# Performance work log

Measured on AMD Instinct MI355X. Metric: run time of the kernel, lower is better.

## Reference

```python
import jax, jax.numpy as jnp
import numpy as np

B, S, H = 8, 2048, 2048


def setup_inputs() -> dict:
    key = jax.random.key(0)
    k1, k2, k3 = jax.random.split(key, 3)
    hidden_state = jax.random.normal(k1, (B, S, H), dtype=jnp.float32)
    attention_mask = jnp.ones((B, S), dtype=jnp.int32)
    special_embeddings_mask = jnp.zeros((B, S), dtype=jnp.int32).at[:, 0].set(1)
    # torch samples -log(Exp(1)) == standard Gumbel; pass noise explicitly for determinism
    gumbel_noise = jax.random.gumbel(k2, (B, S, 2), dtype=jnp.float32)
    W = jax.random.normal(k3, (2 * H, 2), dtype=jnp.float32) / np.sqrt(2.0 * H)
    b = jnp.zeros((2,), dtype=jnp.float32)
    return {"hidden_state": hidden_state, "attention_mask": attention_mask,
            "special_embeddings_mask": special_embeddings_mask,
            "gumbel_noise": gumbel_noise, "W": W, "b": b}


def _forward(hidden_state, W, b, gumbel_noise, attention_mask, special_embeddings_mask):
    Bs, Ss, Hs = hidden_state.shape
    mask_b = attention_mask.astype(bool)
    # adjacent pair features [h_i, h_{i+1}], zero stub appended at the last position
    pairs = jnp.concatenate([hidden_state[:, :-1], hidden_state[:, 1:]], axis=-1)
    pairs = jnp.concatenate([pairs, jnp.zeros((Bs, 1, 2 * Hs), pairs.dtype)], axis=1)
    logits = pairs @ W + b  # [B,S,2]
    # hard Gumbel-softmax with straight-through estimator (tau=1, scale=1, invert=False)
    y_soft = jax.nn.softmax(logits + gumbel_noise, axis=-1)
    index = jnp.argmax(y_soft, axis=-1)
    y_hard = jax.nn.one_hot(index, 2, dtype=logits.dtype)
    mm = y_hard - jax.lax.stop_gradient(y_soft) + y_soft
    # special tokens never merge; padded positions contribute nothing
    mm = jnp.where(special_embeddings_mask.astype(bool)[..., None],
                   jnp.asarray([1.0, 0.0], mm.dtype), mm)
    mm = mm * mask_b[..., None].astype(mm.dtype)
    # ---- vectorized run-length merge (replaces the serial per-batch python loop) ----
    idx = jnp.arange(Ss)
    T = jnp.sum(attention_mask, axis=-1).astype(jnp.int32)  # valid token counts [B]
    valid = idx[None, :] < T[:, None]  # [B,S]
    # a position participates in a merge run iff it votes merge and 1 <= i < T-1
    want = (mm[..., 1] > 0.5) & (idx[None, :] >= 1) & (idx[None, :] < (T[:, None] - 1))
    want_prev = jnp.pad(want[:, :-1], ((0, 0), (1, 0)))
    # new output row starts unless position continues an existing merge run
    inc = (valid & (idx[None, :] >= 1) & ~(want & want_prev)).astype(jnp.int32)
    r = jnp.cumsum(inc, axis=-1)  # destination output row for each input position
    v = jnp.where(want, mm[..., 1], mm[..., 0])
    v = jnp.where(idx[None, :] == 0, jnp.asarray(1.0, v.dtype), v)  # transform[:,0,0] = 1
    v = jnp.where(valid, v, jnp.asarray(0.0, v.dtype))
    b_idx = jnp.arange(Bs)[:, None]
    transform = jnp.zeros((Bs, Ss, Ss), hidden_state.dtype).at[b_idx, r, idx[None, :]].add(v)
    counts = jnp.zeros((Bs, Ss), hidden_state.dtype).at[b_idx, r].add(valid.astype(hidden_state.dtype))
    new_len = r[:, -1] + 1  # merged sequence length per row
    merged_attention_mask = (idx[None, :] < new_len[:, None]).astype(hidden_state.dtype)
    merged_special = jnp.zeros((Bs, Ss), hidden_state.dtype).at[:, 0].set(1.0)
    merged_special = merged_special.at[jnp.arange(Bs), new_len - 1].set(1.0)
    merged_hidden = jnp.einsum('bts,bsh->bth', transform, hidden_state)
    return merged_hidden, merged_attention_mask, merged_special, counts, mm, logits


def reference(hidden_state, attention_mask, special_embeddings_mask, gumbel_noise, W, b):
    return _forward(hidden_state, W, b, gumbel_noise, attention_mask, special_embeddings_mask)
```

## Files before the change

### kernel.cpp

```cpp
#include <hip/hip_runtime.h>
#include <math.h>

#define Bq 8
#define Sq 2048
#define Hq 2048
#define BSq (Bq*Sq)

#define OFF_MH  ((size_t)0)
#define OFF_MAM ((size_t)BSq*Hq)
#define OFF_MSP (OFF_MAM + (size_t)BSq)
#define OFF_CNT (OFF_MSP + (size_t)BSq)
#define OFF_MM  (OFF_CNT + (size_t)BSq)
#define OFF_LG  (OFF_MM + (size_t)2*BSq)

#define WS_DOTS 0
#define WS_V    ((size_t)BSq*16)
#define WS_SEG  (WS_V + (size_t)BSq*4)
#define WS_META (WS_SEG + (size_t)BSq*4)

typedef float nfloat4 __attribute__((ext_vector_type(4)));

__device__ inline float4 f4add(float4 a, float4 b) {
  return make_float4(a.x+b.x, a.y+b.y, a.z+b.z, a.w+b.w);
}

__device__ inline void nt_store_f4(float4 v, float4* p) {
  nfloat4 nv;
  nv.x = v.x; nv.y = v.y; nv.z = v.z; nv.w = v.w;
  __builtin_nontemporal_store(nv, (nfloat4*)p);
}

__global__ __launch_bounds__(256) void k1_dots(const float* __restrict__ hid,
                                               const float* __restrict__ Wg,
                                               float4* __restrict__ dots) {
  __shared__ float4 part[4][256];
  const int tid = threadIdx.x;
  const float4* W4 = (const float4*)Wg;
  const float4 wa0 = W4[2*tid],           wa1 = W4[2*tid+1];
  const float4 wa2 = W4[2*(256+tid)],     wa3 = W4[2*(256+tid)+1];
  const float4 wb0 = W4[1024+2*tid],      wb1 = W4[1024+2*tid+1];
  const float4 wb2 = W4[1024+2*(256+tid)],wb3 = W4[1024+2*(256+tid)+1];
  const int base = blockIdx.x * 16;
  for (int tk0 = 0; tk0 < 16; tk0 += 4) {
    #pragma unroll
    for (int j = 0; j < 4; ++j) {
      const float4* hr = (const float4*)(hid + (size_t)(base + tk0 + j) * Hq);
      float4 h0 = hr[tid], h1 = hr[256+tid];
      float d0 = h0.x*wa0.x + h0.y*wa0.z + h0.z*wa1.x + h0.w*wa1.z
               + h1.x*wa2.x + h1.y*wa2.z + h1.z*wa3.x + h1.w*wa3.z;
      float d1 = h0.x*wa0.y + h0.y*wa0.w + h0.z*wa1.y + h0.w*wa1.w
               + h1.x*wa2.y + h1.y*wa2.w + h1.z*wa3.y + h1.w*wa3.w;
      float e0 = h0.x*wb0.x + h0.y*wb0.z + h0.z*wb1.x + h0.w*wb1.z
               + h1.x*wb2.x + h1.y*wb2.z + h1.z*wb3.x + h1.w*wb3.z;
      float e1 = h0.x*wb0.y + h0.y*wb0.w + h0.z*wb1.y + h0.w*wb1.w
               + h1.x*wb2.y + h1.y*wb2.w + h1.z*wb3.y + h1.w*wb3.w;
      part[j][tid] = make_float4(d0, d1, e0, e1);
    }
    __syncthreads();
    const int w = tid >> 6, l = tid & 63;
    float4 s = f4add(f4add(part[w][l], part[w][l+64]),
                     f4add(part[w][l+128], part[w][l+192]));
    #pragma unroll
    for (int off = 32; off > 0; off >>= 1) {
      s.x += __shfl_xor(s.x, off);
      s.y += __shfl_xor(s.y, off);
      s.z += __shfl_xor(s.z, off);
      s.w += __shfl_xor(s.w, off);
    }
    if (l == 0) dots[base + tk0 + w] = s;
    __syncthreads();
  }
}

__global__ __launch_bounds__(256) void k2_merge(const float4* __restrict__ dots,
                                                const int* __restrict__ attn,
                                                const int* __restrict__ spec,
                                                const float* __restrict__ gum,
                                                const float* __restrict__ bias,
                                                float* __restrict__ out,
                                                float* __restrict__ v_ws,
                                                int* __restrict__ seg_ws,
                                                int* __restrict__ meta) {
  const int b = blockIdx.x, tid = threadIdx.x;
  __shared__ int sums[256];
  __shared__ unsigned char wantL[Sq];
  __shared__ int seg[Sq];
  __shared__ int sT;
  const float b0 = bias[0], b1 = bias[1];

  int tsum = 0;
  #pragma unroll
  for (int k = 0; k < 8; ++k) tsum += attn[b*Sq + tid*8 + k];
  sums[tid] = tsum; __syncthreads();
  for (int off = 128; off > 0; off >>= 1) {
    if (tid < off) sums[tid] += sums[tid+off];
    __syncthreads();
  }
  if (tid == 0) sT = sums[0];
  __syncthreads();
  const int T = sT;

  int wloc[8];
  #pragma unroll
  for (int k = 0; k < 8; ++k) {
    const int i  = tid*8 + k;
    const int gi = b*Sq + i;
    float4 di = dots[gi];
    float l0, l1;
    if (i < Sq-1) {
      float4 dn = dots[gi+1];
      l0 = (di.x + dn.z) + b0;
      l1 = (di.y + dn.w) + b1;
    } else { l0 = b0; l1 = b1; }
    out[OFF_LG + (size_t)gi*2 + 0] = l0;
    out[OFF_LG + (size_t)gi*2 + 1] = l1;
    float z0 = l0 + gum[(size_t)gi*2 + 0];
    float z1 = l1 + gum[(size_t)gi*2 + 1];
    float m  = fmaxf(z0, z1);
    float e0 = expf(z0 - m), e1 = expf(z1 - m);
    float den = e0 + e1;
    float p0 = e0 / den, p1 = e1 / den;
    int idx1 = (p1 > p0) ? 1 : 0;
    float h0f = idx1 ? 0.0f : 1.0f, h1f = idx1 ? 1.0f : 0.0f;
    float mm0 = (h0f - p0) + p0;
    float mm1 = (h1f - p1) + p1;
    if (spec[gi] != 0) { mm0 = 1.0f; mm1 = 0.0f; }
    float am = (float)attn[gi];
    mm0 *= am; mm1 *= am;
    out[OFF_MM + (size_t)gi*2 + 0] = mm0;
    out[OFF_MM + (size_t)gi*2 + 1] = mm1;
    int want = (mm1 > 0.5f) && (i >= 1) && (i < T-1);
    wantL[i] = (unsigned char)want;
    wloc[k]  = want;
    float v = want ? mm1 : mm0;
    if (i == 0) v = 1.0f;
    if (i >= T) v = 0.0f;
    v_ws[gi] = v;
  }
  __syncthreads();

  int incs[8]; int run = 0;
  #pragma unroll
  for (int k = 0; k < 8; ++k) {
    const int i = tid*8 + k;
    int wprev = (i >= 1) ? (int)wantL[i-1] : 0;
    int inc = (i < T && i >= 1 && !(wloc[k] && wprev)) ? 1 : 0;
    run += inc;
    incs[k] = run;
  }
  sums[tid] = run; __syncthreads();
  for (int off = 1; off < 256; off <<= 1) {
    int val = (tid >= off) ? sums[tid - off] : 0;
    __syncthreads();
    sums[tid] += val;
    __syncthreads();
  }
  const int excl = sums[tid] - run;
  const int total = sums[255];

  if (tid == 0) seg[0] = 0;
  #pragma unroll
  for (int k = 0; k < 8; ++k) {
    const int i = tid*8 + k;
    int inc = (k == 0) ? incs[0] : (incs[k] - incs[k-1]);
    if (inc) seg[excl + incs[k]] = i;
  }
  __syncthreads();

  const int nl = total + 1;
  if (tid == 0) { meta[b*2] = nl; meta[b*2+1] = T; }

  #pragma unroll
  for (int k = 0; k < 8; ++k) {
    const int t  = tid*8 + k;
    const int gi = b*Sq + t;
    seg_ws[gi] = (t < nl) ? seg[t] : 0;
    float cnt = 0.0f, mam = 0.0f, msp = 0.0f;
    if (t < nl) {
      int s0 = seg[t];
      int s1 = (t+1 < nl) ? seg[t+1] : T;
      cnt = (float)(s1 - s0);
      mam = 1.0f;
    }
    if (t == 0 || t == nl-1) msp = 1.0f;
    out[OFF_MAM + gi] = mam;
    out[OFF_MSP + gi] = msp;
    out[OFF_CNT + gi] = cnt;
  }
}

#define K3_ROWS 16
__global__ __launch_bounds__(256) void k3_gather(const float* __restrict__ hid,
                                                 const float* __restrict__ v_ws,
                                                 const int* __restrict__ seg_ws,
                                                 const int* __restrict__ meta,
                                                 float* __restrict__ out_mh) {
  const int blocksPerBatch = Sq / K3_ROWS;
  const int b  = blockIdx.x / blocksPerBatch;
  const int t0 = (blockIdx.x % blocksPerBatch) * K3_ROWS;
  const int tid = threadIdx.x;
  const int nl = meta[b*2];
  const int T  = meta[b*2+1];

  __shared__ int bound[K3_ROWS + 1];
  if (tid <= K3_ROWS) {
    const int t = t0 + tid;
    bound[tid] = (t < nl) ? seg_ws[b*Sq + t] : T;
  }
  __syncthreads();

  const int rbase = b*Sq;
  int i = bound[0];
  #pragma unroll 1
  for (int r = 0; r < K3_ROWS; ++r) {
    float4 a0 = make_float4(0.f,0.f,0.f,0.f), a1 = a0;
    const int s1 = bound[r+1];
    for (; i < s1; ++i) {
      const float w = v_ws[rbase + i];
      const float4* hr = (const float4*)(hid + (size_t)(rbase + i) * Hq);
      const float4 x0 = hr[tid];
      const float4 x1 = hr[256 + tid];
      a0.x = fmaf(w, x0.x, a0.x); a0.y = fmaf(w, x0.y, a0.y);
      a0.z = fmaf(w, x0.z, a0.z); a0.w = fmaf(w, x0.w, a0.w);
      a1.x = fmaf(w, x1.x, a1.x); a1.y = fmaf(w, x1.y, a1.y);
      a1.z = fmaf(w, x1.z, a1.z); a1.w = fmaf(w, x1.w, a1.w);
    }
    float4* orow = (float4*)(out_mh + (size_t)(rbase + t0 + r) * Hq);
    nt_store_f4(a0, orow + tid);
    nt_store_f4(a1, orow + 256 + tid);
  }
}

extern "C" void kernel_launch(void* const* d_in, const int* in_sizes, int n_in,
                              void* d_out, int out_size, void* d_ws, size_t ws_size,
                              hipStream_t stream) {
  (void)in_sizes; (void)n_in; (void)out_size; (void)ws_size;
  const float* hid  = (const float*)d_in[0];
  const int*   attn = (const int*)d_in[1];
  const int*   spec = (const int*)d_in[2];
  const float* gum  = (const float*)d_in[3];
  const float* Wg   = (const float*)d_in[4];
  const float* bias = (const float*)d_in[5];
  float* out = (float*)d_out;
  char*  ws  = (char*)d_ws;
  float4* dots  = (float4*)(ws + WS_DOTS);
  float* v_ws   = (float*)(ws + WS_V);
  int*   seg_ws = (int*)(ws + WS_SEG);
  int*   meta   = (int*)(ws + WS_META);

  k1_dots<<<dim3(BSq/16), dim3(256), 0, stream>>>(hid, Wg, dots);
  k2_merge<<<dim3(Bq), dim3(256), 0, stream>>>(dots, attn, spec, gum, bias,
                                               out, v_ws, seg_ws, meta);
  k3_gather<<<dim3(Bq*(Sq/K3_ROWS)), dim3(256), 0, stream>>>(hid, v_ws, seg_ws,
                                                             meta, out + OFF_MH);
}
```

Before: 274.0 us.

## Fuse dots, merge and gather into one cooperative kernel with grid syncs

Turns the three kernels into device phase functions and runs them from a single cooperative kernel of 1024 blocks. Two grid.sync barriers separate the dot, merge and gather phases, which removes two kernel launch boundaries and their drain and refill gaps. In exchange, all 1024 blocks must stay resident (launch_bounds 256,4), and most of them sit idle at the barrier while the 8 merge blocks run. If the cooperative launch fails, it falls back to the original three launches.

```diff
diff --git a/kernel.cpp b/kernel.cpp
--- a/kernel.cpp
+++ b/kernel.cpp
@@ -1,10 +1,15 @@
 #include <hip/hip_runtime.h>
+#include <hip/hip_cooperative_groups.h>
 #include <math.h>
+
+namespace cg = cooperative_groups;
 
 #define Bq 8
 #define Sq 2048
 #define Hq 2048
 #define BSq (Bq*Sq)
+#define GRIDN (BSq/16)
+#define K3_ROWS 16
 
 #define OFF_MH  ((size_t)0)
 #define OFF_MAM ((size_t)BSq*Hq)
@@ -30,17 +35,18 @@
   __builtin_nontemporal_store(nv, (nfloat4*)p);
 }
 
-__global__ __launch_bounds__(256) void k1_dots(const float* __restrict__ hid,
-                                               const float* __restrict__ Wg,
-                                               float4* __restrict__ dots) {
-  __shared__ float4 part[4][256];
-  const int tid = threadIdx.x;
+
+__device__ inline void phase1_dots(int blk, int tid,
+                                   const float* __restrict__ hid,
+                                   const float* __restrict__ Wg,
+                                   float4* __restrict__ dots,
+                                   float4 (*part)[256]) {
   const float4* W4 = (const float4*)Wg;
   const float4 wa0 = W4[2*tid],           wa1 = W4[2*tid+1];
   const float4 wa2 = W4[2*(256+tid)],     wa3 = W4[2*(256+tid)+1];
   const float4 wb0 = W4[1024+2*tid],      wb1 = W4[1024+2*tid+1];
   const float4 wb2 = W4[1024+2*(256+tid)],wb3 = W4[1024+2*(256+tid)+1];
-  const int base = blockIdx.x * 16;
+  const int base = blk * 16;
   for (int tk0 = 0; tk0 < 16; tk0 += 4) {
     #pragma unroll
     for (int j = 0; j < 4; ++j) {
@@ -72,20 +78,18 @@
   }
 }
 
-__global__ __launch_bounds__(256) void k2_merge(const float4* __restrict__ dots,
-                                                const int* __restrict__ attn,
-                                                const int* __restrict__ spec,
-                                                const float* __restrict__ gum,
-                                                const float* __restrict__ bias,
-                                                float* __restrict__ out,
-                                                float* __restrict__ v_ws,
-                                                int* __restrict__ seg_ws,
-                                                int* __restrict__ meta) {
-  const int b = blockIdx.x, tid = threadIdx.x;
-  __shared__ int sums[256];
-  __shared__ unsigned char wantL[Sq];
-  __shared__ int seg[Sq];
-  __shared__ int sT;
+__device__ inline void phase2_merge(int b, int tid,
+                                    const float4* __restrict__ dots,
+                                    const int* __restrict__ attn,
+                                    const int* __restrict__ spec,
+                                    const float* __restrict__ gum,
+                                    const float* __restrict__ bias,
+                                    float* __restrict__ out,
+                                    float* __restrict__ v_ws,
+                                    int* __restrict__ seg_ws,
+                                    int* __restrict__ meta,
+                                    int* sums, unsigned char* wantL, int* seg,
+                                    int* sTp) {
   const float b0 = bias[0], b1 = bias[1];
 
   int tsum = 0;
@@ -96,9 +100,9 @@
     if (tid < off) sums[tid] += sums[tid+off];
     __syncthreads();
   }
-  if (tid == 0) sT = sums[0];
+  if (tid == 0) *sTp = sums[0];
   __syncthreads();
-  const int T = sT;
+  const int T = *sTp;
 
   int wloc[8];
   #pragma unroll
@@ -189,20 +193,19 @@
   }
 }
 
-#define K3_ROWS 16
-__global__ __launch_bounds__(256) void k3_gather(const float* __restrict__ hid,
-                                                 const float* __restrict__ v_ws,
-                                                 const int* __restrict__ seg_ws,
-                                                 const int* __restrict__ meta,
-                                                 float* __restrict__ out_mh) {
+__device__ inline void phase3_gather(int blk, int tid,
+                                     const float* __restrict__ hid,
+                                     const float* __restrict__ v_ws,
+                                     const int* __restrict__ seg_ws,
+                                     const int* __restrict__ meta,
+                                     float* __restrict__ out_mh,
+                                     int* bound) {
   const int blocksPerBatch = Sq / K3_ROWS;
-  const int b  = blockIdx.x / blocksPerBatch;
-  const int t0 = (blockIdx.x % blocksPerBatch) * K3_ROWS;
-  const int tid = threadIdx.x;
+  const int b  = blk / blocksPerBatch;
+  const int t0 = (blk % blocksPerBatch) * K3_ROWS;
   const int nl = meta[b*2];
   const int T  = meta[b*2+1];
 
-  __shared__ int bound[K3_ROWS + 1];
   if (tid <= K3_ROWS) {
     const int t = t0 + tid;
     bound[tid] = (t < nl) ? seg_ws[b*Sq + t] : T;
@@ -231,6 +234,71 @@
   }
 }
 
+__global__ __launch_bounds__(256, 4) void fused_all(
+    const float* __restrict__ hid, const int* __restrict__ attn,
+    const int* __restrict__ spec, const float* __restrict__ gum,
+    const float* __restrict__ Wg, const float* __restrict__ bias,
+    float* __restrict__ out, float4* __restrict__ dots,
+    float* __restrict__ v_ws, int* __restrict__ seg_ws,
+    int* __restrict__ meta) {
+  __shared__ float4 part[4][256];
+  __shared__ int sums[256];
+  __shared__ unsigned char wantL[Sq];
+  __shared__ int seg[Sq];
+  __shared__ int sT;
+  __shared__ int bound[K3_ROWS + 1];
+
+  cg::grid_group grid = cg::this_grid();
+  const int blk = blockIdx.x, tid = threadIdx.x;
+
+  phase1_dots(blk, tid, hid, Wg, dots, part);
+
+  __threadfence();
+  grid.sync();
+
+  if (blk < Bq)
+    phase2_merge(blk, tid, dots, attn, spec, gum, bias, out,
+                 v_ws, seg_ws, meta, sums, wantL, seg, &sT);
+
+  __threadfence();
+  grid.sync();
+
+  phase3_gather(blk, tid, hid, v_ws, seg_ws, meta, out + OFF_MH, bound);
+}
+
+__global__ __launch_bounds__(256) void k1_dots(const float* __restrict__ hid,
+                                               const float* __restrict__ Wg,
+                                               float4* __restrict__ dots) {
+  __shared__ float4 part[4][256];
+  phase1_dots(blockIdx.x, threadIdx.x, hid, Wg, dots, part);
+}
+
+__global__ __launch_bounds__(256) void k2_merge(const float4* __restrict__ dots,
+                                                const int* __restrict__ attn,
+                                                const int* __restrict__ spec,
+                                                const float* __restrict__ gum,
+                                                const float* __restrict__ bias,
+                                                float* __restrict__ out,
+                                                float* __restrict__ v_ws,
+                                                int* __restrict__ seg_ws,
+                                                int* __restrict__ meta) {
+  __shared__ int sums[256];
+  __shared__ unsigned char wantL[Sq];
+  __shared__ int seg[Sq];
+  __shared__ int sT;
+  phase2_merge(blockIdx.x, threadIdx.x, dots, attn, spec, gum, bias, out,
+               v_ws, seg_ws, meta, sums, wantL, seg, &sT);
+}
+
+__global__ __launch_bounds__(256) void k3_gather(const float* __restrict__ hid,
+                                                 const float* __restrict__ v_ws,
+                                                 const int* __restrict__ seg_ws,
+                                                 const int* __restrict__ meta,
+                                                 float* __restrict__ out_mh) {
+  __shared__ int bound[K3_ROWS + 1];
+  phase3_gather(blockIdx.x, threadIdx.x, hid, v_ws, seg_ws, meta, out_mh, bound);
+}
+
 extern "C" void kernel_launch(void* const* d_in, const int* in_sizes, int n_in,
                               void* d_out, int out_size, void* d_ws, size_t ws_size,
                               hipStream_t stream) {
@@ -248,9 +316,17 @@
   int*   seg_ws = (int*)(ws + WS_SEG);
   int*   meta   = (int*)(ws + WS_META);
 
-  k1_dots<<<dim3(BSq/16), dim3(256), 0, stream>>>(hid, Wg, dots);
-  k2_merge<<<dim3(Bq), dim3(256), 0, stream>>>(dots, attn, spec, gum, bias,
-                                               out, v_ws, seg_ws, meta);
-  k3_gather<<<dim3(Bq*(Sq/K3_ROWS)), dim3(256), 0, stream>>>(hid, v_ws, seg_ws,
-                                                             meta, out + OFF_MH);
-}
+  void* kargs[] = { (void*)&hid, (void*)&attn, (void*)&spec, (void*)&gum,
+                    (void*)&Wg, (void*)&bias, (void*)&out, (void*)&dots,
+                    (void*)&v_ws, (void*)&seg_ws, (void*)&meta };
+  hipError_t err = hipLaunchCooperativeKernel((const void*)fused_all,
+                                              dim3(GRIDN), dim3(256),
+                                              kargs, 0, stream);
+  if (err != hipSuccess) {
+    k1_dots<<<dim3(GRIDN), dim3(256), 0, stream>>>(hid, Wg, dots);
+    k2_merge<<<dim3(Bq), dim3(256), 0, stream>>>(dots, attn, spec, gum, bias,
+                                                 out, v_ws, seg_ws, meta);
+    k3_gather<<<dim3(Bq*(Sq/K3_ROWS)), dim3(256), 0, stream>>>(hid, v_ws, seg_ws,
+                                                               meta, out + OFF_MH);
+  }
+}
```

New measurement: 611.6 us. +123.2%, slower.

## Software-pipeline gather loop with two-row lookahead prefetch and halve rows per block

Applied to the files above, without the earlier changes.

Rewrites the merge-gather kernel as a single flattened loop over the block's input rows, keeping the next two hidden rows in registers so their global loads are issued before the current row's FMAs. This targets load-latency stalls from the dependent load-then-accumulate pattern. Rows per block also drop from 16 to 8, doubling the grid for more parallelism. The cost is more registers per thread and extra branching in the loop.

```diff
diff --git a/kernel.cpp b/kernel.cpp
--- a/kernel.cpp
+++ b/kernel.cpp
@@ -5,6 +5,7 @@
 #define Sq 2048
 #define Hq 2048
 #define BSq (Bq*Sq)
+#define K3_ROWS 8
 
 #define OFF_MH  ((size_t)0)
 #define OFF_MAM ((size_t)BSq*Hq)
@@ -189,7 +190,6 @@
   }
 }
 
-#define K3_ROWS 16
 __global__ __launch_bounds__(256) void k3_gather(const float* __restrict__ hid,
                                                  const float* __restrict__ v_ws,
                                                  const int* __restrict__ seg_ws,
@@ -210,24 +210,43 @@
   __syncthreads();
 
   const int rbase = b*Sq;
-  int i = bound[0];
-  #pragma unroll 1
-  for (int r = 0; r < K3_ROWS; ++r) {
-    float4 a0 = make_float4(0.f,0.f,0.f,0.f), a1 = a0;
-    const int s1 = bound[r+1];
-    for (; i < s1; ++i) {
-      const float w = v_ws[rbase + i];
-      const float4* hr = (const float4*)(hid + (size_t)(rbase + i) * Hq);
-      const float4 x0 = hr[tid];
-      const float4 x1 = hr[256 + tid];
-      a0.x = fmaf(w, x0.x, a0.x); a0.y = fmaf(w, x0.y, a0.y);
-      a0.z = fmaf(w, x0.z, a0.z); a0.w = fmaf(w, x0.w, a0.w);
-      a1.x = fmaf(w, x1.x, a1.x); a1.y = fmaf(w, x1.y, a1.y);
-      a1.z = fmaf(w, x1.z, a1.z); a1.w = fmaf(w, x1.w, a1.w);
-    }
-    float4* orow = (float4*)(out_mh + (size_t)(rbase + t0 + r) * Hq);
-    nt_store_f4(a0, orow + tid);
-    nt_store_f4(a1, orow + 256 + tid);
+  const int i0 = bound[0], iN = bound[K3_ROWS];
+
+  const float4 z4 = make_float4(0.f,0.f,0.f,0.f);
+  float4 c0 = z4, c1 = z4, n0 = z4, n1 = z4;
+  float wc = 0.f, wn = 0.f;
+  if (i0 < iN) {
+    const float4* hr = (const float4*)(hid + (size_t)(rbase + i0) * Hq);
+    c0 = hr[tid]; c1 = hr[256 + tid]; wc = v_ws[rbase + i0];
+  }
+  if (i0 + 1 < iN) {
+    const float4* hr = (const float4*)(hid + (size_t)(rbase + i0 + 1) * Hq);
+    n0 = hr[tid]; n1 = hr[256 + tid]; wn = v_ws[rbase + i0 + 1];
+  }
+
+  int i = i0, r = 0;
+  float4 a0 = z4, a1 = z4;
+  while (r < K3_ROWS) {
+    while (r < K3_ROWS && i >= bound[r + 1]) {
+      float4* orow = (float4*)(out_mh + (size_t)(rbase + t0 + r) * Hq);
+      nt_store_f4(a0, orow + tid);
+      nt_store_f4(a1, orow + 256 + tid);
+      a0 = z4; a1 = z4;
+      ++r;
+    }
+    if (r >= K3_ROWS) break;
+    float4 f0 = z4, f1 = z4; float wf = 0.f;
+    if (i + 2 < iN) {
+      const float4* hr = (const float4*)(hid + (size_t)(rbase + i + 2) * Hq);
+      f0 = hr[tid]; f1 = hr[256 + tid]; wf = v_ws[rbase + i + 2];
+    }
+    a0.x = fmaf(wc, c0.x, a0.x); a0.y = fmaf(wc, c0.y, a0.y);
+    a0.z = fmaf(wc, c0.z, a0.z); a0.w = fmaf(wc, c0.w, a0.w);
+    a1.x = fmaf(wc, c1.x, a1.x); a1.y = fmaf(wc, c1.y, a1.y);
+    a1.z = fmaf(wc, c1.z, a1.z); a1.w = fmaf(wc, c1.w, a1.w);
+    c0 = n0; c1 = n1; wc = wn;
+    n0 = f0; n1 = f1; wn = wf;
+    ++i;
   }
 }
 
```

New measurement: 272.0 us. About the same (-0.7%).
